# Kernel optimization log

Hardware: AMD Instinct MI355X
Metric: run time of the kernel (lower is better)

## Reference

```python
import jax, jax.numpy as jnp
import numpy as np

NUM_CLASSES = 19
K = 100                 # max_views_per_class
TEMP = 0.1
BASE_TEMP = 0.07
EPS_NORM = 1e-12


def _l2_normalize(x):
    # matches torch F.normalize(dim=1): x / max(||x||, eps)
    n = jnp.sqrt(jnp.sum(x * x, axis=1, keepdims=True))
    return x / jnp.maximum(n, EPS_NORM)


def _sample_indices(labels_flat):
    # Deterministic per-class sampler: first K pixels of each class.
    # (torch version uses randperm; the downstream math is identical.)
    # Every class is guaranteed >= K pixels by input construction.
    idxs = [jnp.where(labels_flat == c, size=K, fill_value=0)[0]
            for c in range(NUM_CLASSES)]
    return jnp.concatenate(idxs)  # [NUM_CLASSES*K]


def setup_inputs() -> dict:
    key = jax.random.key(0)
    k1, k2, k3, k4 = jax.random.split(key, 4)
    pixel_feats = jax.random.normal(k1, (8, 256, 128, 128), dtype=jnp.float32)
    labels = jax.random.randint(k2, (8, 128, 128), 0, NUM_CLASSES).astype(jnp.int64)
    memory_feats = jax.random.normal(k3, (20000, 256), dtype=jnp.float32)
    memory_labels = jax.random.randint(k4, (20000,), 0, NUM_CLASSES).astype(jnp.int64)
    return {"pixel_feats": pixel_feats, "labels": labels,
            "memory_feats": memory_feats, "memory_labels": memory_labels}


def reference(pixel_feats, labels, memory_feats, memory_labels):
    B, D, H, W = pixel_feats.shape
    feats_flat = pixel_feats.transpose(0, 2, 3, 1).reshape(-1, D)   # [B*H*W, D]
    labels_flat = labels.reshape(-1)

    idx = _sample_indices(labels_flat)
    anchor_feats = feats_flat[idx]                                  # [Na, D]
    anchor_labels = jnp.repeat(jnp.arange(NUM_CLASSES), K)          # [Na]

    contrast_feats = jnp.concatenate([anchor_feats, memory_feats], axis=0)
    contrast_labels = jnp.concatenate([anchor_labels, memory_labels], axis=0)

    a = _l2_normalize(anchor_feats)
    c = _l2_normalize(contrast_feats)
    logits = jnp.einsum('nd,md->nm', a, c) / TEMP                   # [Na, Nc]

    Na, Nc = logits.shape
    mask = (anchor_labels[:, None] == contrast_labels[None, :]).astype(logits.dtype)
    # remove self-contrast (diagonal of the first Na contrast columns)
    rows = jnp.arange(Na)
    logits_mask = jnp.ones((Na, Nc), dtype=logits.dtype).at[rows, rows].set(0.0)
    mask = mask * logits_mask

    exp_logits = jnp.exp(logits) * logits_mask
    log_prob = logits - jnp.log(exp_logits.sum(axis=1, keepdims=True) + 1e-12)

    pos_count = mask.sum(axis=1)                                    # [Na]
    valid = pos_count > 0
    mean_log_prob_pos = (mask * log_prob).sum(axis=1) / jnp.maximum(pos_count, 1.0)
    n_valid = jnp.maximum(jnp.sum(valid).astype(logits.dtype), 1.0)
    loss = -(TEMP / BASE_TEMP) * (jnp.sum(jnp.where(valid, mean_log_prob_pos, 0.0)) / n_valid)
    return loss
```

## Files before the change

### kernel.cpp

```cpp
#include <hip/hip_runtime.h>
#include <hip/hip_bf16.h>
#include <math.h>

#define NCLS   19
#define KPC    100
#define NA     1900
#define NM     20000
#define NC     21900
#define NCP2   22016
#define D      256
#define HW     16384
#define NPIX   131072
#define NBLK   2640

typedef __attribute__((ext_vector_type(8))) short bf16x8;
typedef __attribute__((ext_vector_type(4))) float f32x4;

#define WS_IDX   0
#define WS_ROWS  7680
#define WS_ROWP  15360
#define WS_HIST  23040
#define WS_TKT   23168
#define WS_CLAB  23296
#define WS_CT2   111616

__device__ __forceinline__ short f2bf(float x) {
    __hip_bfloat16 h = __float2bfloat16(x);
    return *(short*)&h;
}

__global__ void sample_kernel(const int* __restrict__ labels, int* __restrict__ idx) {
    const int c = blockIdx.x;
    const int t = threadIdx.x;
    const int wave = t >> 6, lane = t & 63;
    __shared__ int s_base;
    __shared__ int s_wavecnt[4];
    if (t == 0) s_base = 0;
    __syncthreads();
    for (int start = 0; start < NPIX; start += 256) {
        const int i = start + t;
        const bool pred = (labels[i] == c);
        const unsigned long long b = __ballot(pred);
        if (lane == 0) s_wavecnt[wave] = __popcll(b);
        __syncthreads();
        const int base = s_base;
        int wbase = 0;
        for (int w = 0; w < wave; ++w) wbase += s_wavecnt[w];
        const int chunk_total = s_wavecnt[0] + s_wavecnt[1] + s_wavecnt[2] + s_wavecnt[3];
        if (pred) {
            const int rank = base + wbase + __popcll(b & ((1ULL << lane) - 1ULL));
            if (rank < KPC) idx[c * KPC + rank] = i;
        }
        __syncthreads();
        if (t == 0) s_base = base + chunk_total;
        if (base + chunk_total >= KPC) break;
    }
}

__global__ void prep_kernel(const float* __restrict__ mem, const int* __restrict__ memlab,
                            const float* __restrict__ pixel, const int* __restrict__ idx,
                            float* rowS, float* rowP, int* clab, int* hist, int* ticket,
                            short* __restrict__ Ct2) {
    const int b = blockIdx.x, t = threadIdx.x;
    if (b < 2500) {
        const int r = b * 8 + (t >> 5);
        const int kq = t & 31;
        const float4 v0 = *(const float4*)(mem + (size_t)r * D + kq * 8);
        const float4 v1 = *(const float4*)(mem + (size_t)r * D + kq * 8 + 4);
        float ssq = v0.x*v0.x + v0.y*v0.y + v0.z*v0.z + v0.w*v0.w
                  + v1.x*v1.x + v1.y*v1.y + v1.z*v1.z + v1.w*v1.w;
        #pragma unroll
        for (int o = 16; o; o >>= 1) ssq += __shfl_xor(ssq, o, 32);
        const float inv = 1.0f / fmaxf(sqrtf(ssq), 1e-12f);
        bf16x8 outv;
        outv[0] = f2bf(v0.x * inv); outv[1] = f2bf(v0.y * inv);
        outv[2] = f2bf(v0.z * inv); outv[3] = f2bf(v0.w * inv);
        outv[4] = f2bf(v1.x * inv); outv[5] = f2bf(v1.y * inv);
        outv[6] = f2bf(v1.z * inv); outv[7] = f2bf(v1.w * inv);
        *(bf16x8*)(Ct2 + ((size_t)kq * NCP2 + NA + r) * 8) = outv;
    } else if (b < 2586) {
        const int i = (b - 2500) * 256 + t;
        clab[i] = (i < NA) ? ((i * 5243) >> 19)
                           : ((i < NC) ? memlab[i - NA] : -1);
        if (i < 1920) { rowS[i] = 0.f; rowP[i] = 0.f; }
        if (i < 32 * (NCP2 - NC)) {
            const int kq = i / (NCP2 - NC);
            const int n  = NC + (i - kq * (NCP2 - NC));
            bf16x8 z = {};
            *(bf16x8*)(Ct2 + ((size_t)kq * NCP2 + n) * 8) = z;
        }
    } else if (b == 2586) {
        __shared__ int h[NCLS];
        if (t < NCLS) h[t] = 0;
        if (t == 32) *ticket = 0;
        __syncthreads();
        for (int i = t; i < NM; i += 256) atomicAdd(&h[memlab[i]], 1);
        __syncthreads();
        if (t < NCLS) hist[t] = h[t];
    } else {
        const int a = (b - 2587) * 8 + (t >> 5);
        const int kq = t & 31;
        if (a >= NA) return;
        const int p = idx[a];
        const int bb = p >> 14;
        const int hw = p & (HW - 1);
        const float* base = pixel + ((size_t)(bb * D + kq * 8)) * HW + hw;
        float v[8];
        float ssq = 0.f;
        #pragma unroll
        for (int jj = 0; jj < 8; ++jj) { v[jj] = base[(size_t)jj * HW]; ssq += v[jj] * v[jj]; }
        #pragma unroll
        for (int o = 16; o; o >>= 1) ssq += __shfl_xor(ssq, o, 32);
        const float inv = 1.0f / fmaxf(sqrtf(ssq), 1e-12f);
        bf16x8 outv;
        #pragma unroll
        for (int jj = 0; jj < 8; ++jj) outv[jj] = f2bf(v[jj] * inv);
        *(bf16x8*)(Ct2 + ((size_t)kq * NCP2 + a) * 8) = outv;
    }
}

__global__ __launch_bounds__(256, 3)
void gemm_kernel(const short* __restrict__ Ct2, const int* __restrict__ clab,
                 float* __restrict__ rowS, float* __restrict__ rowP,
                 const int* __restrict__ hist, int* ticket, float* __restrict__ out) {
    __shared__ __align__(16) short As[8 * 128 * 8];
    __shared__ __align__(16) short Bs[8 * 128 * 8];
    __shared__ int flag;
    __shared__ float rs[4];
    const int tid  = threadIdx.x;
    const int lane = tid & 63;
    const int w    = tid >> 6;
    const int wn   = w >> 1, wm = w & 1;
    const int quad = lane >> 4, l16 = lane & 15;

    const int L   = blockIdx.x;
    const int xcd = L & 7;
    const int j   = L >> 3;
    const int m_t = j % 15;
    const int nl  = j / 15;
    const int cnt = (xcd < 4) ? 22 : 21;
    const int nst = (xcd < 4) ? xcd * 22 : 88 + (xcd - 4) * 21;

    if (nl < cnt) {
        const int m0 = m_t * 128;
        const int n0 = (nst + nl) * 128;
        f32x4 acc[4][4] = {};

        for (int kc = 0; kc < 4; ++kc) {
            #pragma unroll
            for (int i = 0; i < 4; ++i) {
                const int c    = w * 4 + i;
                const int kq   = c >> 1;
                const int half = (c & 1) * 64;
                const int kqg  = kc * 8 + kq;
                __builtin_amdgcn_global_load_lds(
                    (const __attribute__((address_space(1))) void*)(Ct2 + ((size_t)kqg * NCP2 + n0 + half + lane) * 8),
                    (__attribute__((address_space(3))) void*)(As + (size_t)(kq * 128 + half + lane) * 8),
                    16, 0, 0);
                __builtin_amdgcn_global_load_lds(
                    (const __attribute__((address_space(1))) void*)(Ct2 + ((size_t)kqg * NCP2 + m0 + half + lane) * 8),
                    (__attribute__((address_space(3))) void*)(Bs + (size_t)(kq * 128 + half + lane) * 8),
                    16, 0, 0);
            }
            __syncthreads();
            #pragma unroll
            for (int ks = 0; ks < 2; ++ks) {
                const int kqb = ks * 4 + quad;
                bf16x8 af[4], bfm[4];
                #pragma unroll
                for (int ni = 0; ni < 4; ++ni)
                    af[ni] = *(const bf16x8*)(As + (size_t)(kqb * 128 + wn * 64 + ni * 16 + l16) * 8);
                #pragma unroll
                for (int mi = 0; mi < 4; ++mi)
                    bfm[mi] = *(const bf16x8*)(Bs + (size_t)(kqb * 128 + wm * 64 + mi * 16 + l16) * 8);
                #pragma unroll
                for (int mi = 0; mi < 4; ++mi)
                    #pragma unroll
                    for (int ni = 0; ni < 4; ++ni)
                        acc[mi][ni] = __builtin_amdgcn_mfma_f32_16x16x32_bf16(
                            af[ni], bfm[mi], acc[mi][ni], 0, 0, 0);
            }
            __syncthreads();
        }

        const int nbase = n0 + wn * 64 + quad * 4;
        int labv[16];
        #pragma unroll
        for (int ni = 0; ni < 4; ++ni)
            #pragma unroll
            for (int r = 0; r < 4; ++r)
                labv[ni * 4 + r] = clab[nbase + ni * 16 + r];
        #pragma unroll
        for (int mi = 0; mi < 4; ++mi) {
            const int m    = m0 + wm * 64 + mi * 16 + l16;
            const int mlab = (m * 5243) >> 19;
            float s = 0.f, p = 0.f;
            #pragma unroll
            for (int ni = 0; ni < 4; ++ni)
                #pragma unroll
                for (int r = 0; r < 4; ++r) {
                    const int n  = nbase + ni * 16 + r;
                    const int lv = labv[ni * 4 + r];
                    const float l = acc[mi][ni][r] * 10.0f;
                    if (lv >= 0 && n != m) {
                        s += __expf(l);
                        if (lv == mlab) p += l;
                    }
                }
            s += __shfl_xor(s, 16, 64); s += __shfl_xor(s, 32, 64);
            p += __shfl_xor(p, 16, 64); p += __shfl_xor(p, 32, 64);
            if (quad == 0 && m < NA) {
                atomicAdd(&rowS[m], s);
                atomicAdd(&rowP[m], p);
            }
        }
    }

    __syncthreads();
    if (tid == 0) {
        __threadfence();
        flag = (atomicAdd(ticket, 1) == NBLK - 1) ? 1 : 0;
    }
    __syncthreads();
    if (flag) {
        __threadfence();
        float sum = 0.f;
        for (int n = tid; n < NA; n += 256) {
            const int cls = (n * 5243) >> 19;
            const float cntf = 99.0f + (float)hist[cls];
            const float logS = logf(rowS[n] + 1e-12f);
            sum += (rowP[n] - cntf * logS) / cntf;
        }
        #pragma unroll
        for (int o = 32; o; o >>= 1) sum += __shfl_xor(sum, o, 64);
        if (lane == 0) rs[w] = sum;
        __syncthreads();
        if (tid == 0) out[0] = -(10.0f / 7.0f) * ((rs[0] + rs[1] + rs[2] + rs[3]) / 1900.0f);
    }
}

extern "C" void kernel_launch(void* const* d_in, const int* in_sizes, int n_in,
                              void* d_out, int out_size, void* d_ws, size_t ws_size,
                              hipStream_t stream) {
    const float* pixel  = (const float*)d_in[0];
    const int*   labels = (const int*)d_in[1];
    const float* mem    = (const float*)d_in[2];
    const int*   memlab = (const int*)d_in[3];
    char* ws = (char*)d_ws;
    int*   idx  = (int*)(ws + WS_IDX);
    float* rowS = (float*)(ws + WS_ROWS);
    float* rowP = (float*)(ws + WS_ROWP);
    int*   hist = (int*)(ws + WS_HIST);
    int*   tkt  = (int*)(ws + WS_TKT);
    int*   clab = (int*)(ws + WS_CLAB);
    short* Ct2  = (short*)(ws + WS_CT2);
    float* out  = (float*)d_out;

    sample_kernel<<<dim3(NCLS), dim3(256), 0, stream>>>(labels, idx);
    prep_kernel<<<dim3(2825), dim3(256), 0, stream>>>(mem, memlab, pixel, idx,
                                                      rowS, rowP, clab, hist, tkt, Ct2);
    gemm_kernel<<<dim3(NBLK), dim3(256), 0, stream>>>(Ct2, clab, rowS, rowP, hist, tkt, out);
}
```

Measured before the change: 275.8 us.

## Fuse sampling with gather, keep anchor tile in registers, split out finalize

The sampler now gathers and normalizes its own anchor pixels, so the index buffer and that part of the prep kernel go away. The GEMM now holds the full-K anchor (m) fragments in registers, reloads only the contrast tile through LDS, and processes two n-tiles per block, with half as many blocks and launch bounds lowered to 2. The ticket-based last-block reduction becomes a separate single-block finalize kernel. This cuts redundant anchor loads and the atomic ticket, at the cost of much higher register pressure, lower occupancy and an extra launch.

Measured after the change: 287.6 us. +4.3%, slower.

```diff
diff --git a/kernel.cpp b/kernel.cpp
--- a/kernel.cpp
+++ b/kernel.cpp
@@ -11,16 +11,13 @@
 #define D      256
 #define HW     16384
 #define NPIX   131072
-#define NBLK   2640
 
 typedef __attribute__((ext_vector_type(8))) short bf16x8;
 typedef __attribute__((ext_vector_type(4))) float f32x4;
 
-#define WS_IDX   0
 #define WS_ROWS  7680
 #define WS_ROWP  15360
 #define WS_HIST  23040
-#define WS_TKT   23168
 #define WS_CLAB  23296
 #define WS_CT2   111616
 
@@ -29,10 +26,13 @@
     return *(short*)&h;
 }
 
-__global__ void sample_kernel(const int* __restrict__ labels, int* __restrict__ idx) {
+__global__ void sample_gather_kernel(const int* __restrict__ labels,
+                                     const float* __restrict__ pixel,
+                                     short* __restrict__ Ct2) {
     const int c = blockIdx.x;
     const int t = threadIdx.x;
     const int wave = t >> 6, lane = t & 63;
+    __shared__ int s_idx[KPC];
     __shared__ int s_base;
     __shared__ int s_wavecnt[4];
     if (t == 0) s_base = 0;
@@ -49,17 +49,35 @@
         const int chunk_total = s_wavecnt[0] + s_wavecnt[1] + s_wavecnt[2] + s_wavecnt[3];
         if (pred) {
             const int rank = base + wbase + __popcll(b & ((1ULL << lane) - 1ULL));
-            if (rank < KPC) idx[c * KPC + rank] = i;
+            if (rank < KPC) s_idx[rank] = i;
         }
         __syncthreads();
         if (t == 0) s_base = base + chunk_total;
         if (base + chunk_total >= KPC) break;
     }
+    __syncthreads();
+    const int slot = t >> 5, kq = t & 31;
+    for (int r = slot; r < KPC; r += 8) {
+        const int p = s_idx[r];
+        const int b = p >> 14;
+        const int hw = p & (HW - 1);
+        const float* base = pixel + ((size_t)(b * D + kq * 8)) * HW + hw;
+        float v[8];
+        float ssq = 0.f;
+        #pragma unroll
+        for (int j = 0; j < 8; ++j) { v[j] = base[(size_t)j * HW]; ssq += v[j] * v[j]; }
+        #pragma unroll
+        for (int o = 16; o; o >>= 1) ssq += __shfl_xor(ssq, o, 32);
+        const float inv = 1.0f / fmaxf(sqrtf(ssq), 1e-12f);
+        bf16x8 outv;
+        #pragma unroll
+        for (int j = 0; j < 8; ++j) outv[j] = f2bf(v[j] * inv);
+        *(bf16x8*)(Ct2 + ((size_t)kq * NCP2 + c * KPC + r) * 8) = outv;
+    }
 }
 
 __global__ void prep_kernel(const float* __restrict__ mem, const int* __restrict__ memlab,
-                            const float* __restrict__ pixel, const int* __restrict__ idx,
-                            float* rowS, float* rowP, int* clab, int* hist, int* ticket,
+                            float* rowS, float* rowP, int* clab, int* hist,
                             short* __restrict__ Ct2) {
     const int b = blockIdx.x, t = threadIdx.x;
     if (b < 2500) {
@@ -89,44 +107,20 @@
             bf16x8 z = {};
             *(bf16x8*)(Ct2 + ((size_t)kq * NCP2 + n) * 8) = z;
         }
-    } else if (b == 2586) {
+    } else {
         __shared__ int h[NCLS];
         if (t < NCLS) h[t] = 0;
-        if (t == 32) *ticket = 0;
         __syncthreads();
         for (int i = t; i < NM; i += 256) atomicAdd(&h[memlab[i]], 1);
         __syncthreads();
         if (t < NCLS) hist[t] = h[t];
-    } else {
-        const int a = (b - 2587) * 8 + (t >> 5);
-        const int kq = t & 31;
-        if (a >= NA) return;
-        const int p = idx[a];
-        const int bb = p >> 14;
-        const int hw = p & (HW - 1);
-        const float* base = pixel + ((size_t)(bb * D + kq * 8)) * HW + hw;
-        float v[8];
-        float ssq = 0.f;
-        #pragma unroll
-        for (int jj = 0; jj < 8; ++jj) { v[jj] = base[(size_t)jj * HW]; ssq += v[jj] * v[jj]; }
-        #pragma unroll
-        for (int o = 16; o; o >>= 1) ssq += __shfl_xor(ssq, o, 32);
-        const float inv = 1.0f / fmaxf(sqrtf(ssq), 1e-12f);
-        bf16x8 outv;
-        #pragma unroll
-        for (int jj = 0; jj < 8; ++jj) outv[jj] = f2bf(v[jj] * inv);
-        *(bf16x8*)(Ct2 + ((size_t)kq * NCP2 + a) * 8) = outv;
-    }
-}
-
-__global__ __launch_bounds__(256, 3)
+    }
+}
+
+__global__ __launch_bounds__(256, 2)
 void gemm_kernel(const short* __restrict__ Ct2, const int* __restrict__ clab,
-                 float* __restrict__ rowS, float* __restrict__ rowP,
-                 const int* __restrict__ hist, int* ticket, float* __restrict__ out) {
+                 float* __restrict__ rowS, float* __restrict__ rowP) {
     __shared__ __align__(16) short As[8 * 128 * 8];
-    __shared__ __align__(16) short Bs[8 * 128 * 8];
-    __shared__ int flag;
-    __shared__ float rs[4];
     const int tid  = threadIdx.x;
     const int lane = tid & 63;
     const int w    = tid >> 6;
@@ -137,48 +131,50 @@
     const int xcd = L & 7;
     const int j   = L >> 3;
     const int m_t = j % 15;
-    const int nl  = j / 15;
-    const int cnt = (xcd < 4) ? 22 : 21;
-    const int nst = (xcd < 4) ? xcd * 22 : 88 + (xcd - 4) * 21;
-
-    if (nl < cnt) {
-        const int m0 = m_t * 128;
-        const int n0 = (nst + nl) * 128;
+    const int gl  = j / 15;
+    const int gcnt = (xcd < 6) ? 11 : 10;
+    if (gl >= gcnt) return;
+    const int g   = (xcd < 6) ? xcd * 11 + gl : 66 + (xcd - 6) * 10 + gl;
+    const int m0  = m_t * 128;
+
+    bf16x8 Bfr[8][4];
+    {
+        const int mb = m0 + wm * 64 + l16;
+        #pragma unroll
+        for (int q = 0; q < 8; ++q)
+            #pragma unroll
+            for (int mi = 0; mi < 4; ++mi)
+                Bfr[q][mi] = *(const bf16x8*)(Ct2 + ((size_t)(q * 4 + quad) * NCP2 + mb + mi * 16) * 8);
+    }
+
+    for (int t2 = 0; t2 < 2; ++t2) {
+        const int n0 = g * 256 + t2 * 128;
         f32x4 acc[4][4] = {};
 
         for (int kc = 0; kc < 4; ++kc) {
             #pragma unroll
             for (int i = 0; i < 4; ++i) {
-                const int c    = w * 4 + i;
-                const int kq   = c >> 1;
-                const int half = (c & 1) * 64;
-                const int kqg  = kc * 8 + kq;
+                const int cc   = w * 4 + i;
+                const int kql  = cc >> 1;
+                const int half = (cc & 1) * 64;
                 __builtin_amdgcn_global_load_lds(
-                    (const __attribute__((address_space(1))) void*)(Ct2 + ((size_t)kqg * NCP2 + n0 + half + lane) * 8),
-                    (__attribute__((address_space(3))) void*)(As + (size_t)(kq * 128 + half + lane) * 8),
-                    16, 0, 0);
-                __builtin_amdgcn_global_load_lds(
-                    (const __attribute__((address_space(1))) void*)(Ct2 + ((size_t)kqg * NCP2 + m0 + half + lane) * 8),
-                    (__attribute__((address_space(3))) void*)(Bs + (size_t)(kq * 128 + half + lane) * 8),
+                    (const __attribute__((address_space(1))) void*)(Ct2 + ((size_t)(kc * 8 + kql) * NCP2 + n0 + half + lane) * 8),
+                    (__attribute__((address_space(3))) void*)(As + (size_t)(kql * 128 + half + lane) * 8),
                     16, 0, 0);
             }
             __syncthreads();
             #pragma unroll
             for (int ks = 0; ks < 2; ++ks) {
-                const int kqb = ks * 4 + quad;
-                bf16x8 af[4], bfm[4];
+                bf16x8 af[4];
                 #pragma unroll
                 for (int ni = 0; ni < 4; ++ni)
-                    af[ni] = *(const bf16x8*)(As + (size_t)(kqb * 128 + wn * 64 + ni * 16 + l16) * 8);
-                #pragma unroll
-                for (int mi = 0; mi < 4; ++mi)
-                    bfm[mi] = *(const bf16x8*)(Bs + (size_t)(kqb * 128 + wm * 64 + mi * 16 + l16) * 8);
+                    af[ni] = *(const bf16x8*)(As + (size_t)((ks * 4 + quad) * 128 + wn * 64 + ni * 16 + l16) * 8);
                 #pragma unroll
                 for (int mi = 0; mi < 4; ++mi)
                     #pragma unroll
                     for (int ni = 0; ni < 4; ++ni)
                         acc[mi][ni] = __builtin_amdgcn_mfma_f32_16x16x32_bf16(
-                            af[ni], bfm[mi], acc[mi][ni], 0, 0, 0);
+                            af[ni], Bfr[kc * 2 + ks][mi], acc[mi][ni], 0, 0, 0);
             }
             __syncthreads();
         }
@@ -215,28 +211,25 @@
             }
         }
     }
-
+}
+
+__global__ void finalize_kernel(const float* __restrict__ rowS, const float* __restrict__ rowP,
+                                const int* __restrict__ hist, float* __restrict__ out) {
+    const int t = threadIdx.x;
+    float sum = 0.f;
+    for (int n = t; n < NA; n += 256) {
+        const int cls = (n * 5243) >> 19;
+        const float cnt = 99.0f + (float)hist[cls];
+        const float logS = logf(rowS[n] + 1e-12f);
+        sum += (rowP[n] - cnt * logS) / cnt;
+    }
+    #pragma unroll
+    for (int o = 32; o; o >>= 1) sum += __shfl_xor(sum, o, 64);
+    __shared__ float rs[4];
+    if ((t & 63) == 0) rs[t >> 6] = sum;
     __syncthreads();
-    if (tid == 0) {
-        __threadfence();
-        flag = (atomicAdd(ticket, 1) == NBLK - 1) ? 1 : 0;
-    }
-    __syncthreads();
-    if (flag) {
-        __threadfence();
-        float sum = 0.f;
-        for (int n = tid; n < NA; n += 256) {
-            const int cls = (n * 5243) >> 19;
-            const float cntf = 99.0f + (float)hist[cls];
-            const float logS = logf(rowS[n] + 1e-12f);
-            sum += (rowP[n] - cntf * logS) / cntf;
-        }
-        #pragma unroll
-        for (int o = 32; o; o >>= 1) sum += __shfl_xor(sum, o, 64);
-        if (lane == 0) rs[w] = sum;
-        __syncthreads();
-        if (tid == 0) out[0] = -(10.0f / 7.0f) * ((rs[0] + rs[1] + rs[2] + rs[3]) / 1900.0f);
-    }
+    if (t == 0)
+        out[0] = -(10.0f / 7.0f) * ((rs[0] + rs[1] + rs[2] + rs[3]) / 1900.0f);
 }
 
 extern "C" void kernel_launch(void* const* d_in, const int* in_sizes, int n_in,
@@ -247,17 +240,15 @@
     const float* mem    = (const float*)d_in[2];
     const int*   memlab = (const int*)d_in[3];
     char* ws = (char*)d_ws;
-    int*   idx  = (int*)(ws + WS_IDX);
     float* rowS = (float*)(ws + WS_ROWS);
     float* rowP = (float*)(ws + WS_ROWP);
     int*   hist = (int*)(ws + WS_HIST);
-    int*   tkt  = (int*)(ws + WS_TKT);
     int*   clab = (int*)(ws + WS_CLAB);
     short* Ct2  = (short*)(ws + WS_CT2);
     float* out  = (float*)d_out;
 
-    sample_kernel<<<dim3(NCLS), dim3(256), 0, stream>>>(labels, idx);
-    prep_kernel<<<dim3(2825), dim3(256), 0, stream>>>(mem, memlab, pixel, idx,
-                                                      rowS, rowP, clab, hist, tkt, Ct2);
-    gemm_kernel<<<dim3(NBLK), dim3(256), 0, stream>>>(Ct2, clab, rowS, rowP, hist, tkt, out);
-}
+    sample_gather_kernel<<<dim3(NCLS), dim3(256), 0, stream>>>(labels, pixel, Ct2);
+    prep_kernel<<<dim3(2587), dim3(256), 0, stream>>>(mem, memlab, rowS, rowP, clab, hist, Ct2);
+    gemm_kernel<<<dim3(1320), dim3(256), 0, stream>>>(Ct2, clab, rowS, rowP);
+    finalize_kernel<<<dim3(1), dim3(256), 0, stream>>>(rowS, rowP, hist, out);
+}
```
